# Kernel optimization log

Measured on AMD Instinct MI355X. Metric: run time of the kernel, lower is better.

The kernel has to match this reference:

```python
import jax, jax.numpy as jnp
import numpy as np

EPS = 1e-12


def _phi(e):
    # e: [C, L] -> pairwise euclidean distances [C, C], diagonal zeroed
    sq = jnp.sum(e * e, axis=1)                      # [C]
    prod = e @ e.T                                   # [C, C]
    d2 = sq[:, None] + sq[None, :] - 2.0 * prod
    d = jnp.sqrt(jnp.clip(d2, EPS, None))
    C = e.shape[0]
    return d * (1.0 - jnp.eye(C, dtype=e.dtype))


def setup_inputs() -> dict:
    key = jax.random.key(0)
    k1, k2, k3 = jax.random.split(key, 3)
    N, C, L = 64, 512, 256
    le_student = jax.random.normal(k1, (N, C, L), dtype=jnp.float32)
    le_teacher = jax.random.normal(k2, (N, C, L), dtype=jnp.float32)
    targets = jax.random.randint(k3, (N, C), 0, 2, dtype=jnp.int32)
    return {"le_student": le_student, "le_teacher": le_teacher, "targets": targets}


def reference(le_student, le_teacher, targets):
    N, C, L = le_student.shape
    m = targets.astype(le_student.dtype)             # [N, C] 0/1 mask
    es = le_student * m[:, :, None]                  # zero out negative rows
    et = le_teacher * m[:, :, None]

    Ds = jax.vmap(_phi)(es)                          # [N, C, C]
    Dt = jax.vmap(_phi)(et)                          # [N, C, C]

    eye = jnp.eye(C, dtype=m.dtype)
    pm = m[:, :, None] * m[:, None, :]               # pairs of positive rows
    offdiag = pm * (1.0 - eye)                       # off-diagonal positive pairs

    npos = jnp.sum(m, axis=1)                        # [N]
    cnt = npos * (npos - 1.0)                        # entries with d > 0 in submatrix
    valid = npos > 1.0
    safe_cnt = jnp.maximum(cnt, 1.0)

    mean_s = jnp.sum(Ds * offdiag, axis=(1, 2)) / safe_cnt
    mean_t = jax.lax.stop_gradient(jnp.sum(Dt * offdiag, axis=(1, 2)) / safe_cnt)
    mean_s = jnp.where(valid, mean_s, 1.0)
    mean_t = jnp.where(valid, mean_t, 1.0)

    d = Ds / mean_s[:, None, None]
    td = jax.lax.stop_gradient(Dt / mean_t[:, None, None])

    diff = d - td
    adiff = jnp.abs(diff)
    huber = jnp.where(adiff < 1.0, 0.5 * diff * diff, adiff - 0.5)

    per = jnp.sum(huber * pm, axis=(1, 2)) / jnp.maximum(npos, 1.0)
    return jnp.sum(jnp.where(valid, per, 0.0))
```

## Files before the change

kernel.cpp:

```cpp
#include <hip/hip_runtime.h>
#include <hip/hip_bf16.h>
#include <hip/hip_fp16.h>
#include <math.h>

#define NB 64
#define CC 512
#define LL 256

typedef __attribute__((ext_vector_type(4))) float floatx4;
typedef __attribute__((ext_vector_type(8))) short short8;

static __device__ __forceinline__ unsigned f2bf2(float x, float y) {
    __hip_bfloat162 h = __float22bfloat162_rn(make_float2(x, y));
    union { __hip_bfloat162 h; unsigned u; } c; c.h = h;
    return c.u;
}
static __device__ __forceinline__ unsigned f2h(float x) {
    __half h = __float2half_rn(x);
    union { __half h; unsigned short u; } c; c.h = h;
    return (unsigned)c.u;
}
static __device__ __forceinline__ float h2f(unsigned u) {
    union { unsigned short u; __half h; } c; c.u = (unsigned short)u;
    return __half2float(c.h);
}

__global__ __launch_bounds__(256) void dist_kernel(
    const float* __restrict__ S, const float* __restrict__ T,
    const int* __restrict__ targets,
    float* __restrict__ psumS, float* __restrict__ psumT,
    int* __restrict__ npos_ws, unsigned* __restrict__ D,
    float* __restrict__ out)
{
    const int bx = blockIdx.x;
    const int n = bx & (NB - 1), lin = bx >> 6;
    int tI = 0, rem = lin;
    while (rem >= 8 - tI) { rem -= 8 - tI; ++tI; }
    const int tJ = tI + rem;
    const bool diag = (tI == tJ);

    __shared__ int s_idx[CC];
    __shared__ int s_cnt[8], s_off[8];
    __shared__ int s_npS;
    __shared__ __align__(16) unsigned short lds[4][64][40];
    __shared__ float s_norm[4][64];
    __shared__ float redA[4], redB[4];

    const int tid = threadIdx.x;
    const int w = tid >> 6, lane = tid & 63;

    const int* tg = targets + n * CC;
    const bool p0 = tg[tid] != 0;
    const bool p1 = tg[tid + 256] != 0;
    const unsigned long long m0 = __ballot(p0);
    const unsigned long long m1 = __ballot(p1);
    if (lane == 0) { s_cnt[w] = __popcll(m0); s_cnt[4 + w] = __popcll(m1); }
    __syncthreads();
    if (tid == 0) {
        int a = 0;
        for (int i = 0; i < 8; ++i) { s_off[i] = a; a += s_cnt[i]; }
        s_npS = a;
    }
    __syncthreads();
    const unsigned long long below = (1ull << lane) - 1ull;
    if (p0) s_idx[s_off[w] + __popcll(m0 & below)] = tid;
    if (p1) s_idx[s_off[4 + w] + __popcll(m1 & below)] = tid + 256;
    __syncthreads();
    const int np = s_npS;

    if (tid == 0 && lin == 0) {
        npos_ws[n] = np;
        if (n == 0) out[0] = 0.0f;
    }

    const bool work = (np >= 2) && (tI * 64 < np) && (tJ * 64 < np);

    float t0 = 0.0f, t1 = 0.0f;
    if (work) {
        const bool stager = (!diag) || ((w & 1) == 0);
        const char* Pbase = (const char*)(((w >> 1) ? T : S) + (size_t)n * CC * LL);
        const int tileBase = ((w & 1) ? tJ : tI) * 64;
        const int r8 = lane >> 3, c8 = lane & 7;
        unsigned off_[8];
        #pragma unroll
        for (int i = 0; i < 8; ++i) {
            const int gk = tileBase + r8 + 8 * i;
            const int row = s_idx[(gk < np) ? gk : 0];
            off_[i] = (unsigned)(row * LL * 4 + c8 * 16);
        }

        float4 pre[8];
        float nprt[8];
        #pragma unroll
        for (int i = 0; i < 8; ++i) nprt[i] = 0.0f;
        if (stager) {
            #pragma unroll
            for (int i = 0; i < 8; ++i) pre[i] = *(const float4*)(Pbase + off_[i]);
        }

        const int m16 = lane & 15, quad = lane >> 4;
        const int bufB = diag ? 0 : 1;
        const int wrow = w * 16;

        floatx4 accS[4], accT[4];
        #pragma unroll
        for (int c = 0; c < 4; ++c) {
            accS[c][0] = 0; accS[c][1] = 0; accS[c][2] = 0; accS[c][3] = 0;
            accT[c][0] = 0; accT[c][1] = 0; accT[c][2] = 0; accT[c][3] = 0;
        }

        for (int kk = 0; kk < 8; ++kk) {
            __syncthreads();
            if (stager) {
                #pragma unroll
                for (int i = 0; i < 8; ++i) {
                    nprt[i] += pre[i].x * pre[i].x + pre[i].y * pre[i].y +
                               pre[i].z * pre[i].z + pre[i].w * pre[i].w;
                    *(uint2*)&lds[w][r8 + 8 * i][c8 * 4] =
                        make_uint2(f2bf2(pre[i].x, pre[i].y), f2bf2(pre[i].z, pre[i].w));
                }
            }
            __syncthreads();
            if (stager && kk < 7) {
                #pragma unroll
                for (int i = 0; i < 8; ++i)
                    pre[i] = *(const float4*)(Pbase + off_[i] + (kk + 1) * 128);
            }
            const int aoff = (wrow + m16) * 40 + quad * 8;
            const short8 a_s = *(const short8*)(&lds[0][0][0] + aoff);
            const short8 a_t = *(const short8*)(&lds[2][0][0] + aoff);
            #pragma unroll
            for (int c = 0; c < 4; ++c) {
                const int boff = (c * 16 + m16) * 40 + quad * 8;
                const short8 b_s = *(const short8*)(&lds[bufB][0][0] + boff);
                const short8 b_t = *(const short8*)(&lds[2 + bufB][0][0] + boff);
                accS[c] = __builtin_amdgcn_mfma_f32_16x16x32_bf16(a_s, b_s, accS[c], 0, 0, 0);
                accT[c] = __builtin_amdgcn_mfma_f32_16x16x32_bf16(a_t, b_t, accT[c], 0, 0, 0);
            }
        }

        if (stager) {
            #pragma unroll
            for (int i = 0; i < 8; ++i) {
                float v = nprt[i];
                v += __shfl_xor(v, 1); v += __shfl_xor(v, 2); v += __shfl_xor(v, 4);
                if (c8 == 0) s_norm[w][r8 + 8 * i] = v;
            }
        }
        __syncthreads();

        unsigned* Dn = D + ((size_t)bx << 12);
        float l0 = 0.0f, l1 = 0.0f;
        #pragma unroll
        for (int c = 0; c < 4; ++c) {
            const int colL = c * 16 + m16;
            const int gj = tJ * 64 + colL;
            const float nBs = s_norm[bufB][colL];
            const float nBt = s_norm[2 + bufB][colL];
            #pragma unroll
            for (int r = 0; r < 4; ++r) {
                const int rowL = wrow + quad * 4 + r;
                const int gi = tI * 64 + rowL;
                const float ds = sqrtf(fmaxf(s_norm[0][rowL] + nBs - 2.0f * accS[c][r], 1e-12f));
                const float dt = sqrtf(fmaxf(s_norm[2][rowL] + nBt - 2.0f * accT[c][r], 1e-12f));
                if (gi < np && gj < np && gi != gj) { l0 += ds; l1 += dt; }
                Dn[rowL * 64 + colL] = f2h(ds) | (f2h(dt) << 16);
            }
        }

        #pragma unroll
        for (int o = 32; o; o >>= 1) { l0 += __shfl_down(l0, o); l1 += __shfl_down(l1, o); }
        if (lane == 0) { redA[w] = l0; redB[w] = l1; }
        __syncthreads();
        if (tid == 0) {
            const float wgt = diag ? 1.0f : 2.0f;
            t0 = wgt * (redA[0] + redA[1] + redA[2] + redA[3]);
            t1 = wgt * (redB[0] + redB[1] + redB[2] + redB[3]);
        }
    }
    if (tid == 0) { psumS[bx] = t0; psumT[bx] = t1; }
}

__global__ __launch_bounds__(256) void huber_kernel(
    const unsigned* __restrict__ D, const int* __restrict__ npos,
    const float* __restrict__ psumS, const float* __restrict__ psumT,
    float* __restrict__ out)
{
    const int bx = blockIdx.x;
    const int n = bx & (NB - 1), lin = bx >> 6;
    int tI = 0, rem = lin;
    while (rem >= 8 - tI) { rem -= 8 - tI; ++tI; }
    const int tJ = tI + rem;

    const int np = npos[n];
    if (np < 2) return;
    if (tI * 64 >= np || tJ * 64 >= np) return;

    float ss = 0.0f, st = 0.0f;
    #pragma unroll
    for (int t = 0; t < 36; ++t) { ss += psumS[t * 64 + n]; st += psumT[t * 64 + n]; }
    const float cnt = (float)np * (float)(np - 1);
    const float inv_ms = cnt / ss;
    const float inv_mt = cnt / st;

    const uint4* Dn = (const uint4*)(D + ((size_t)bx << 12));
    const int tid = threadIdx.x;

    float h = 0.0f;
    #pragma unroll
    for (int it = 0; it < 4; ++it) {
        const int e4 = it * 256 + tid;
        const uint4 v = Dn[e4];
        const unsigned vv[4] = { v.x, v.y, v.z, v.w };
        const int e0 = e4 * 4;
        #pragma unroll
        for (int k = 0; k < 4; ++k) {
            const int e = e0 + k;
            const int gi = tI * 64 + (e >> 6);
            const int gj = tJ * 64 + (e & 63);
            if (gi < np && gj < np && gi != gj) {
                const float ds = h2f(vv[k] & 0xffffu);
                const float dt = h2f(vv[k] >> 16);
                const float diff = ds * inv_ms - dt * inv_mt;
                const float ad = fabsf(diff);
                h += (ad < 1.0f) ? 0.5f * diff * diff : ad - 0.5f;
            }
        }
    }

    #pragma unroll
    for (int o = 32; o; o >>= 1) h += __shfl_down(h, o);
    __shared__ float red[4];
    const int w = tid >> 6, lane = tid & 63;
    if (lane == 0) red[w] = h;
    __syncthreads();
    if (tid == 0) {
        const float wgt = (tI == tJ) ? 1.0f : 2.0f;
        atomicAdd(out, wgt * (red[0] + red[1] + red[2] + red[3]) / (float)np);
    }
}

extern "C" void kernel_launch(void* const* d_in, const int* in_sizes, int n_in,
                              void* d_out, int out_size, void* d_ws, size_t ws_size,
                              hipStream_t stream) {
    const float* S = (const float*)d_in[0];
    const float* T = (const float*)d_in[1];
    const int* targets = (const int*)d_in[2];
    float* out = (float*)d_out;

    float* psumS = (float*)d_ws;
    float* psumT = psumS + 2304;
    int* npos_ws = (int*)(psumT + 2304);
    size_t off = ((size_t)((char*)(npos_ws + 64) - (char*)d_ws) + 255) & ~(size_t)255;
    unsigned* D = (unsigned*)((char*)d_ws + off);

    dist_kernel<<<NB * 36, 256, 0, stream>>>(S, T, targets, psumS, psumT, npos_ws, D, out);
    huber_kernel<<<NB * 36, 256, 0, stream>>>(D, npos_ws, psumS, psumT, out);
}
```

Before: 133.3 us.

## Add prep pass compacting positive rows to bf16 and use smaller 32x32 tiles

A new prep kernel gathers the positive rows, converts them to a packed bf16 array, and precomputes row norms once per batch. The distance kernel then reads operands for 32x32 tiles straight from global memory with one wave per block, instead of restaging fp32 rows into LDS for every 64x64 tile. Per-batch mean sums now accumulate through atomics rather than a partial-sum array scan. The price is an extra launch, a round trip of the compacted bf16 copy through memory, and four times as many smaller blocks.

```diff
diff --git a/kernel.cpp b/kernel.cpp
--- a/kernel.cpp
+++ b/kernel.cpp
@@ -25,26 +25,18 @@
     return __half2float(c.h);
 }
 
-__global__ __launch_bounds__(256) void dist_kernel(
+__global__ __launch_bounds__(256) void prep_kernel(
     const float* __restrict__ S, const float* __restrict__ T,
     const int* __restrict__ targets,
-    float* __restrict__ psumS, float* __restrict__ psumT,
-    int* __restrict__ npos_ws, unsigned* __restrict__ D,
-    float* __restrict__ out)
+    int* __restrict__ idx, int* __restrict__ npos,
+    float* __restrict__ sumS, float* __restrict__ sumT, float* __restrict__ out,
+    unsigned short* __restrict__ Ps, unsigned short* __restrict__ Pt,
+    float* __restrict__ ns, float* __restrict__ nt)
 {
-    const int bx = blockIdx.x;
-    const int n = bx & (NB - 1), lin = bx >> 6;
-    int tI = 0, rem = lin;
-    while (rem >= 8 - tI) { rem -= 8 - tI; ++tI; }
-    const int tJ = tI + rem;
-    const bool diag = (tI == tJ);
-
+    const int g = blockIdx.x, n = blockIdx.y;
     __shared__ int s_idx[CC];
     __shared__ int s_cnt[8], s_off[8];
     __shared__ int s_npS;
-    __shared__ __align__(16) unsigned short lds[4][64][40];
-    __shared__ float s_norm[4][64];
-    __shared__ float redA[4], redB[4];
 
     const int tid = threadIdx.x;
     const int w = tid >> 6, lane = tid & 63;
@@ -68,156 +60,172 @@
     __syncthreads();
     const int np = s_npS;
 
-    if (tid == 0 && lin == 0) {
-        npos_ws[n] = np;
-        if (n == 0) out[0] = 0.0f;
-    }
-
-    const bool work = (np >= 2) && (tI * 64 < np) && (tJ * 64 < np);
-
-    float t0 = 0.0f, t1 = 0.0f;
-    if (work) {
-        const bool stager = (!diag) || ((w & 1) == 0);
-        const char* Pbase = (const char*)(((w >> 1) ? T : S) + (size_t)n * CC * LL);
-        const int tileBase = ((w & 1) ? tJ : tI) * 64;
-        const int r8 = lane >> 3, c8 = lane & 7;
-        unsigned off_[8];
-        #pragma unroll
-        for (int i = 0; i < 8; ++i) {
-            const int gk = tileBase + r8 + 8 * i;
-            const int row = s_idx[(gk < np) ? gk : 0];
-            off_[i] = (unsigned)(row * LL * 4 + c8 * 16);
-        }
-
-        float4 pre[8];
-        float nprt[8];
-        #pragma unroll
-        for (int i = 0; i < 8; ++i) nprt[i] = 0.0f;
-        if (stager) {
-            #pragma unroll
-            for (int i = 0; i < 8; ++i) pre[i] = *(const float4*)(Pbase + off_[i]);
-        }
-
-        const int m16 = lane & 15, quad = lane >> 4;
-        const int bufB = diag ? 0 : 1;
-        const int wrow = w * 16;
-
-        floatx4 accS[4], accT[4];
-        #pragma unroll
-        for (int c = 0; c < 4; ++c) {
-            accS[c][0] = 0; accS[c][1] = 0; accS[c][2] = 0; accS[c][3] = 0;
-            accT[c][0] = 0; accT[c][1] = 0; accT[c][2] = 0; accT[c][3] = 0;
-        }
-
-        for (int kk = 0; kk < 8; ++kk) {
-            __syncthreads();
-            if (stager) {
-                #pragma unroll
-                for (int i = 0; i < 8; ++i) {
-                    nprt[i] += pre[i].x * pre[i].x + pre[i].y * pre[i].y +
-                               pre[i].z * pre[i].z + pre[i].w * pre[i].w;
-                    *(uint2*)&lds[w][r8 + 8 * i][c8 * 4] =
-                        make_uint2(f2bf2(pre[i].x, pre[i].y), f2bf2(pre[i].z, pre[i].w));
-                }
-            }
-            __syncthreads();
-            if (stager && kk < 7) {
-                #pragma unroll
-                for (int i = 0; i < 8; ++i)
-                    pre[i] = *(const float4*)(Pbase + off_[i] + (kk + 1) * 128);
-            }
-            const int aoff = (wrow + m16) * 40 + quad * 8;
-            const short8 a_s = *(const short8*)(&lds[0][0][0] + aoff);
-            const short8 a_t = *(const short8*)(&lds[2][0][0] + aoff);
-            #pragma unroll
-            for (int c = 0; c < 4; ++c) {
-                const int boff = (c * 16 + m16) * 40 + quad * 8;
-                const short8 b_s = *(const short8*)(&lds[bufB][0][0] + boff);
-                const short8 b_t = *(const short8*)(&lds[2 + bufB][0][0] + boff);
-                accS[c] = __builtin_amdgcn_mfma_f32_16x16x32_bf16(a_s, b_s, accS[c], 0, 0, 0);
-                accT[c] = __builtin_amdgcn_mfma_f32_16x16x32_bf16(a_t, b_t, accT[c], 0, 0, 0);
-            }
-        }
-
-        if (stager) {
-            #pragma unroll
-            for (int i = 0; i < 8; ++i) {
-                float v = nprt[i];
-                v += __shfl_xor(v, 1); v += __shfl_xor(v, 2); v += __shfl_xor(v, 4);
-                if (c8 == 0) s_norm[w][r8 + 8 * i] = v;
-            }
-        }
-        __syncthreads();
-
-        unsigned* Dn = D + ((size_t)bx << 12);
-        float l0 = 0.0f, l1 = 0.0f;
-        #pragma unroll
-        for (int c = 0; c < 4; ++c) {
-            const int colL = c * 16 + m16;
-            const int gj = tJ * 64 + colL;
-            const float nBs = s_norm[bufB][colL];
-            const float nBt = s_norm[2 + bufB][colL];
+    if (g == 0) {
+        for (int k = tid; k < np; k += 256) idx[n * CC + k] = s_idx[k];
+        if (tid == 0) {
+            npos[n] = np;
+            sumS[n] = 0.0f; sumT[n] = 0.0f;
+            if (n == 0) out[0] = 0.0f;
+        }
+    }
+
+    const int kend = min(np, (g + 1) * 64);
+    for (int k = g * 64 + w; k < kend; k += 4) {
+        const int r = s_idx[k];
+        const float4 a = ((const float4*)(S + ((size_t)n * CC + r) * LL))[lane];
+        const float4 b = ((const float4*)(T + ((size_t)n * CC + r) * LL))[lane];
+        const size_t dst = ((size_t)n * CC + k) * LL + lane * 4;
+        *(uint2*)&Ps[dst] = make_uint2(f2bf2(a.x, a.y), f2bf2(a.z, a.w));
+        *(uint2*)&Pt[dst] = make_uint2(f2bf2(b.x, b.y), f2bf2(b.z, b.w));
+        float vs = a.x * a.x + a.y * a.y + a.z * a.z + a.w * a.w;
+        float vt = b.x * b.x + b.y * b.y + b.z * b.z + b.w * b.w;
+        #pragma unroll
+        for (int o = 32; o; o >>= 1) { vs += __shfl_down(vs, o); vt += __shfl_down(vt, o); }
+        if (lane == 0) { ns[n * CC + k] = vs; nt[n * CC + k] = vt; }
+    }
+}
+
+__global__ __launch_bounds__(64) void dist_kernel(
+    const unsigned short* __restrict__ Ps, const unsigned short* __restrict__ Pt,
+    const float* __restrict__ ns, const float* __restrict__ nt,
+    const int* __restrict__ npos,
+    float* __restrict__ sumS, float* __restrict__ sumT,
+    unsigned* __restrict__ D)
+{
+    const int bx = blockIdx.x;
+    const int n = bx & (NB - 1), lin = bx >> 6;
+    int tI = 0, rem = lin;
+    while (rem >= 16 - tI) { rem -= 16 - tI; ++tI; }
+    const int tJ = tI + rem;
+    const bool diag = (tI == tJ);
+
+    const int np = npos[n];
+    if (np < 2 || tI * 32 >= np || tJ * 32 >= np) return;
+
+    const int lane = threadIdx.x;
+    const int m16 = lane & 15, quad = lane >> 4;
+
+    const int rA0 = min(tI * 32 + m16, np - 1);
+    const int rA1 = min(tI * 32 + 16 + m16, np - 1);
+    const int rB0 = min(tJ * 32 + m16, np - 1);
+    const int rB1 = min(tJ * 32 + 16 + m16, np - 1);
+    const size_t base = (size_t)n * CC * LL + quad * 8;
+    const unsigned short* a0s = Ps + base + (size_t)rA0 * LL;
+    const unsigned short* a1s = Ps + base + (size_t)rA1 * LL;
+    const unsigned short* b0s = Ps + base + (size_t)rB0 * LL;
+    const unsigned short* b1s = Ps + base + (size_t)rB1 * LL;
+    const unsigned short* a0t = Pt + base + (size_t)rA0 * LL;
+    const unsigned short* a1t = Pt + base + (size_t)rA1 * LL;
+    const unsigned short* b0t = Pt + base + (size_t)rB0 * LL;
+    const unsigned short* b1t = Pt + base + (size_t)rB1 * LL;
+
+    floatx4 accS[4], accT[4];
+    #pragma unroll
+    for (int q = 0; q < 4; ++q) {
+        accS[q][0] = 0; accS[q][1] = 0; accS[q][2] = 0; accS[q][3] = 0;
+        accT[q][0] = 0; accT[q][1] = 0; accT[q][2] = 0; accT[q][3] = 0;
+    }
+
+    #pragma unroll 2
+    for (int kk = 0; kk < 8; ++kk) {
+        const int o = kk * 32;
+        const short8 fa0s = *(const short8*)(a0s + o);
+        const short8 fa1s = *(const short8*)(a1s + o);
+        const short8 fb0s = *(const short8*)(b0s + o);
+        const short8 fb1s = *(const short8*)(b1s + o);
+        const short8 fa0t = *(const short8*)(a0t + o);
+        const short8 fa1t = *(const short8*)(a1t + o);
+        const short8 fb0t = *(const short8*)(b0t + o);
+        const short8 fb1t = *(const short8*)(b1t + o);
+        accS[0] = __builtin_amdgcn_mfma_f32_16x16x32_bf16(fa0s, fb0s, accS[0], 0, 0, 0);
+        accS[1] = __builtin_amdgcn_mfma_f32_16x16x32_bf16(fa0s, fb1s, accS[1], 0, 0, 0);
+        accS[2] = __builtin_amdgcn_mfma_f32_16x16x32_bf16(fa1s, fb0s, accS[2], 0, 0, 0);
+        accS[3] = __builtin_amdgcn_mfma_f32_16x16x32_bf16(fa1s, fb1s, accS[3], 0, 0, 0);
+        accT[0] = __builtin_amdgcn_mfma_f32_16x16x32_bf16(fa0t, fb0t, accT[0], 0, 0, 0);
+        accT[1] = __builtin_amdgcn_mfma_f32_16x16x32_bf16(fa0t, fb1t, accT[1], 0, 0, 0);
+        accT[2] = __builtin_amdgcn_mfma_f32_16x16x32_bf16(fa1t, fb0t, accT[2], 0, 0, 0);
+        accT[3] = __builtin_amdgcn_mfma_f32_16x16x32_bf16(fa1t, fb1t, accT[3], 0, 0, 0);
+    }
+
+    float nsR[8], ntR[8];
+    #pragma unroll
+    for (int qi = 0; qi < 2; ++qi)
+        #pragma unroll
+        for (int r = 0; r < 4; ++r) {
+            const int gi = min(tI * 32 + qi * 16 + quad * 4 + r, np - 1);
+            nsR[qi * 4 + r] = ns[n * CC + gi];
+            ntR[qi * 4 + r] = nt[n * CC + gi];
+        }
+    float nsC[2], ntC[2];
+    #pragma unroll
+    for (int qj = 0; qj < 2; ++qj) {
+        const int gj = min(tJ * 32 + qj * 16 + m16, np - 1);
+        nsC[qj] = ns[n * CC + gj];
+        ntC[qj] = nt[n * CC + gj];
+    }
+
+    unsigned* Dn = D + ((size_t)bx << 10);
+    float l0 = 0.0f, l1 = 0.0f;
+    #pragma unroll
+    for (int qi = 0; qi < 2; ++qi)
+        #pragma unroll
+        for (int qj = 0; qj < 2; ++qj) {
+            const int q = qi * 2 + qj;
+            const int colL = qj * 16 + m16;
+            const int gj = tJ * 32 + colL;
             #pragma unroll
             for (int r = 0; r < 4; ++r) {
-                const int rowL = wrow + quad * 4 + r;
-                const int gi = tI * 64 + rowL;
-                const float ds = sqrtf(fmaxf(s_norm[0][rowL] + nBs - 2.0f * accS[c][r], 1e-12f));
-                const float dt = sqrtf(fmaxf(s_norm[2][rowL] + nBt - 2.0f * accT[c][r], 1e-12f));
+                const int rowL = qi * 16 + quad * 4 + r;
+                const int gi = tI * 32 + rowL;
+                const float ds = sqrtf(fmaxf(nsR[qi * 4 + r] + nsC[qj] - 2.0f * accS[q][r], 1e-12f));
+                const float dt = sqrtf(fmaxf(ntR[qi * 4 + r] + ntC[qj] - 2.0f * accT[q][r], 1e-12f));
                 if (gi < np && gj < np && gi != gj) { l0 += ds; l1 += dt; }
-                Dn[rowL * 64 + colL] = f2h(ds) | (f2h(dt) << 16);
+                Dn[rowL * 32 + colL] = f2h(ds) | (f2h(dt) << 16);
             }
         }
 
-        #pragma unroll
-        for (int o = 32; o; o >>= 1) { l0 += __shfl_down(l0, o); l1 += __shfl_down(l1, o); }
-        if (lane == 0) { redA[w] = l0; redB[w] = l1; }
-        __syncthreads();
-        if (tid == 0) {
-            const float wgt = diag ? 1.0f : 2.0f;
-            t0 = wgt * (redA[0] + redA[1] + redA[2] + redA[3]);
-            t1 = wgt * (redB[0] + redB[1] + redB[2] + redB[3]);
-        }
-    }
-    if (tid == 0) { psumS[bx] = t0; psumT[bx] = t1; }
-}
-
-__global__ __launch_bounds__(256) void huber_kernel(
+    #pragma unroll
+    for (int o = 32; o; o >>= 1) { l0 += __shfl_down(l0, o); l1 += __shfl_down(l1, o); }
+    if (lane == 0) {
+        const float wgt = diag ? 1.0f : 2.0f;
+        atomicAdd(&sumS[n], wgt * l0);
+        atomicAdd(&sumT[n], wgt * l1);
+    }
+}
+
+__global__ __launch_bounds__(64) void huber_kernel(
     const unsigned* __restrict__ D, const int* __restrict__ npos,
-    const float* __restrict__ psumS, const float* __restrict__ psumT,
+    const float* __restrict__ sumS, const float* __restrict__ sumT,
     float* __restrict__ out)
 {
     const int bx = blockIdx.x;
     const int n = bx & (NB - 1), lin = bx >> 6;
     int tI = 0, rem = lin;
-    while (rem >= 8 - tI) { rem -= 8 - tI; ++tI; }
+    while (rem >= 16 - tI) { rem -= 16 - tI; ++tI; }
     const int tJ = tI + rem;
 
     const int np = npos[n];
-    if (np < 2) return;
-    if (tI * 64 >= np || tJ * 64 >= np) return;
-
-    float ss = 0.0f, st = 0.0f;
-    #pragma unroll
-    for (int t = 0; t < 36; ++t) { ss += psumS[t * 64 + n]; st += psumT[t * 64 + n]; }
+    if (np < 2 || tI * 32 >= np || tJ * 32 >= np) return;
+
     const float cnt = (float)np * (float)(np - 1);
-    const float inv_ms = cnt / ss;
-    const float inv_mt = cnt / st;
-
-    const uint4* Dn = (const uint4*)(D + ((size_t)bx << 12));
-    const int tid = threadIdx.x;
+    const float inv_ms = cnt / sumS[n];
+    const float inv_mt = cnt / sumT[n];
+
+    const uint4* Dn = (const uint4*)(D + ((size_t)bx << 10));
+    const int lane = threadIdx.x;
 
     float h = 0.0f;
     #pragma unroll
     for (int it = 0; it < 4; ++it) {
-        const int e4 = it * 256 + tid;
+        const int e4 = it * 64 + lane;
         const uint4 v = Dn[e4];
         const unsigned vv[4] = { v.x, v.y, v.z, v.w };
         const int e0 = e4 * 4;
         #pragma unroll
         for (int k = 0; k < 4; ++k) {
             const int e = e0 + k;
-            const int gi = tI * 64 + (e >> 6);
-            const int gj = tJ * 64 + (e & 63);
+            const int gi = tI * 32 + (e >> 5);
+            const int gj = tJ * 32 + (e & 31);
             if (gi < np && gj < np && gi != gj) {
                 const float ds = h2f(vv[k] & 0xffffu);
                 const float dt = h2f(vv[k] >> 16);
@@ -230,13 +238,9 @@
 
     #pragma unroll
     for (int o = 32; o; o >>= 1) h += __shfl_down(h, o);
-    __shared__ float red[4];
-    const int w = tid >> 6, lane = tid & 63;
-    if (lane == 0) red[w] = h;
-    __syncthreads();
-    if (tid == 0) {
+    if (lane == 0) {
         const float wgt = (tI == tJ) ? 1.0f : 2.0f;
-        atomicAdd(out, wgt * (red[0] + red[1] + red[2] + red[3]) / (float)np);
+        atomicAdd(out, wgt * h / (float)np);
     }
 }
 
@@ -248,12 +252,21 @@
     const int* targets = (const int*)d_in[2];
     float* out = (float*)d_out;
 
-    float* psumS = (float*)d_ws;
-    float* psumT = psumS + 2304;
-    int* npos_ws = (int*)(psumT + 2304);
-    size_t off = ((size_t)((char*)(npos_ws + 64) - (char*)d_ws) + 255) & ~(size_t)255;
-    unsigned* D = (unsigned*)((char*)d_ws + off);
-
-    dist_kernel<<<NB * 36, 256, 0, stream>>>(S, T, targets, psumS, psumT, npos_ws, D, out);
-    huber_kernel<<<NB * 36, 256, 0, stream>>>(D, npos_ws, psumS, psumT, out);
-}
+    char* p = (char*)d_ws;
+    int* idx = (int*)p;                  p += (size_t)NB * CC * 4;
+    int* npos = (int*)p;                 p += NB * 4;
+    float* sumS = (float*)p;             p += NB * 4;
+    float* sumT = (float*)p;             p += NB * 4;
+    float* ns = (float*)p;               p += (size_t)NB * CC * 4;
+    float* nt = (float*)p;               p += (size_t)NB * CC * 4;
+    p = (char*)(((size_t)p + 255) & ~(size_t)255);
+    unsigned short* Ps = (unsigned short*)p;  p += (size_t)NB * CC * LL * 2;
+    unsigned short* Pt = (unsigned short*)p;  p += (size_t)NB * CC * LL * 2;
+    unsigned* D = (unsigned*)p;
+
+    prep_kernel<<<dim3(8, NB), 256, 0, stream>>>(S, T, targets, idx, npos,
+                                                 sumS, sumT, out, Ps, Pt, ns, nt);
+    const int nblk = 136 * NB;
+    dist_kernel<<<nblk, 64, 0, stream>>>(Ps, Pt, ns, nt, npos, sumS, sumT, D);
+    huber_kernel<<<nblk, 64, 0, stream>>>(D, npos, sumS, sumT, out);
+}
```

Result: slower. 177.4 us (+33.1%).

## Split index compaction into prep kernel, double-buffer LDS, use atomic per-sample sums

Applied to the files above, without the earlier changes.

Moves the per-sample positive-row compaction out of every dist block into a small prep kernel that writes indices to global memory. Dist blocks are now grouped per sample and tiles beyond the positive count exit early through a tile decode on the actual tile count. The LDS staging becomes double-buffered, which drops one barrier per k-step. Per-sample distance sums are accumulated with atomics instead of partial arrays summed in the huber kernel. The cost is an extra kernel launch, more LDS per block, and nondeterministic float atomic ordering.

```diff
diff --git a/kernel.cpp b/kernel.cpp
--- a/kernel.cpp
+++ b/kernel.cpp
@@ -25,30 +25,14 @@
     return __half2float(c.h);
 }
 
-__global__ __launch_bounds__(256) void dist_kernel(
-    const float* __restrict__ S, const float* __restrict__ T,
+__global__ __launch_bounds__(256) void prep_kernel(
     const int* __restrict__ targets,
-    float* __restrict__ psumS, float* __restrict__ psumT,
-    int* __restrict__ npos_ws, unsigned* __restrict__ D,
-    float* __restrict__ out)
+    int* __restrict__ idx, int* __restrict__ npos,
+    float* __restrict__ sumS, float* __restrict__ sumT, float* __restrict__ out)
 {
-    const int bx = blockIdx.x;
-    const int n = bx & (NB - 1), lin = bx >> 6;
-    int tI = 0, rem = lin;
-    while (rem >= 8 - tI) { rem -= 8 - tI; ++tI; }
-    const int tJ = tI + rem;
-    const bool diag = (tI == tJ);
-
-    __shared__ int s_idx[CC];
+    const int n = blockIdx.x, tid = threadIdx.x;
     __shared__ int s_cnt[8], s_off[8];
-    __shared__ int s_npS;
-    __shared__ __align__(16) unsigned short lds[4][64][40];
-    __shared__ float s_norm[4][64];
-    __shared__ float redA[4], redB[4];
-
-    const int tid = threadIdx.x;
     const int w = tid >> 6, lane = tid & 63;
-
     const int* tg = targets + n * CC;
     const bool p0 = tg[tid] != 0;
     const bool p1 = tg[tid + 256] != 0;
@@ -59,149 +43,162 @@
     if (tid == 0) {
         int a = 0;
         for (int i = 0; i < 8; ++i) { s_off[i] = a; a += s_cnt[i]; }
-        s_npS = a;
+        npos[n] = a;
+        sumS[n] = 0.0f; sumT[n] = 0.0f;
+        if (n == 0) out[0] = 0.0f;
     }
     __syncthreads();
     const unsigned long long below = (1ull << lane) - 1ull;
-    if (p0) s_idx[s_off[w] + __popcll(m0 & below)] = tid;
-    if (p1) s_idx[s_off[4 + w] + __popcll(m1 & below)] = tid + 256;
-    __syncthreads();
-    const int np = s_npS;
-
-    if (tid == 0 && lin == 0) {
-        npos_ws[n] = np;
-        if (n == 0) out[0] = 0.0f;
-    }
-
-    const bool work = (np >= 2) && (tI * 64 < np) && (tJ * 64 < np);
-
-    float t0 = 0.0f, t1 = 0.0f;
-    if (work) {
-        const bool stager = (!diag) || ((w & 1) == 0);
-        const char* Pbase = (const char*)(((w >> 1) ? T : S) + (size_t)n * CC * LL);
-        const int tileBase = ((w & 1) ? tJ : tI) * 64;
-        const int r8 = lane >> 3, c8 = lane & 7;
-        unsigned off_[8];
-        #pragma unroll
-        for (int i = 0; i < 8; ++i) {
-            const int gk = tileBase + r8 + 8 * i;
-            const int row = s_idx[(gk < np) ? gk : 0];
-            off_[i] = (unsigned)(row * LL * 4 + c8 * 16);
-        }
-
-        float4 pre[8];
-        float nprt[8];
-        #pragma unroll
-        for (int i = 0; i < 8; ++i) nprt[i] = 0.0f;
-        if (stager) {
-            #pragma unroll
-            for (int i = 0; i < 8; ++i) pre[i] = *(const float4*)(Pbase + off_[i]);
-        }
-
-        const int m16 = lane & 15, quad = lane >> 4;
-        const int bufB = diag ? 0 : 1;
-        const int wrow = w * 16;
-
-        floatx4 accS[4], accT[4];
-        #pragma unroll
-        for (int c = 0; c < 4; ++c) {
-            accS[c][0] = 0; accS[c][1] = 0; accS[c][2] = 0; accS[c][3] = 0;
-            accT[c][0] = 0; accT[c][1] = 0; accT[c][2] = 0; accT[c][3] = 0;
-        }
-
-        for (int kk = 0; kk < 8; ++kk) {
-            __syncthreads();
-            if (stager) {
-                #pragma unroll
-                for (int i = 0; i < 8; ++i) {
-                    nprt[i] += pre[i].x * pre[i].x + pre[i].y * pre[i].y +
-                               pre[i].z * pre[i].z + pre[i].w * pre[i].w;
-                    *(uint2*)&lds[w][r8 + 8 * i][c8 * 4] =
-                        make_uint2(f2bf2(pre[i].x, pre[i].y), f2bf2(pre[i].z, pre[i].w));
-                }
-            }
-            __syncthreads();
-            if (stager && kk < 7) {
-                #pragma unroll
-                for (int i = 0; i < 8; ++i)
-                    pre[i] = *(const float4*)(Pbase + off_[i] + (kk + 1) * 128);
-            }
-            const int aoff = (wrow + m16) * 40 + quad * 8;
-            const short8 a_s = *(const short8*)(&lds[0][0][0] + aoff);
-            const short8 a_t = *(const short8*)(&lds[2][0][0] + aoff);
-            #pragma unroll
-            for (int c = 0; c < 4; ++c) {
-                const int boff = (c * 16 + m16) * 40 + quad * 8;
-                const short8 b_s = *(const short8*)(&lds[bufB][0][0] + boff);
-                const short8 b_t = *(const short8*)(&lds[2 + bufB][0][0] + boff);
-                accS[c] = __builtin_amdgcn_mfma_f32_16x16x32_bf16(a_s, b_s, accS[c], 0, 0, 0);
-                accT[c] = __builtin_amdgcn_mfma_f32_16x16x32_bf16(a_t, b_t, accT[c], 0, 0, 0);
-            }
-        }
-
+    if (p0) idx[n * CC + s_off[w] + __popcll(m0 & below)] = tid;
+    if (p1) idx[n * CC + s_off[4 + w] + __popcll(m1 & below)] = tid + 256;
+}
+
+static __device__ __forceinline__ bool decode_tile(int t, int u, int& tI, int& tJ) {
+    if (t >= (u * (u + 1)) >> 1) return false;
+    tI = 0;
+    while (t >= u - tI) { t -= u - tI; ++tI; }
+    tJ = tI + t;
+    return true;
+}
+
+__global__ __launch_bounds__(256) void dist_kernel(
+    const float* __restrict__ S, const float* __restrict__ T,
+    const int* __restrict__ idx, const int* __restrict__ npos,
+    float* __restrict__ sumS, float* __restrict__ sumT,
+    unsigned* __restrict__ D)
+{
+    const int bx = blockIdx.x;
+    const int n = bx / 36;
+    const int np = npos[n];
+    if (np < 2) return;
+    int tI, tJ;
+    if (!decode_tile(bx - n * 36, (np + 63) >> 6, tI, tJ)) return;
+    const bool diag = (tI == tJ);
+
+    __shared__ __align__(16) unsigned short lds[4][2][64][40];
+    __shared__ float s_norm[4][64];
+    __shared__ float redA[4], redB[4];
+
+    const int tid = threadIdx.x;
+    const int w = tid >> 6, lane = tid & 63;
+
+    const bool stager = (!diag) || ((w & 1) == 0);
+    const char* Pbase = (const char*)(((w >> 1) ? T : S) + (size_t)n * CC * LL);
+    const int tileBase = ((w & 1) ? tJ : tI) * 64;
+    const int r8 = lane >> 3, c8 = lane & 7;
+    unsigned off_[8];
+    #pragma unroll
+    for (int i = 0; i < 8; ++i) {
+        const int gk = tileBase + r8 + 8 * i;
+        const int row = idx[n * CC + ((gk < np) ? gk : 0)];
+        off_[i] = (unsigned)(row * LL * 4 + c8 * 16);
+    }
+
+    float4 pre[8];
+    float nprt[8];
+    #pragma unroll
+    for (int i = 0; i < 8; ++i) nprt[i] = 0.0f;
+    if (stager) {
+        #pragma unroll
+        for (int i = 0; i < 8; ++i) pre[i] = *(const float4*)(Pbase + off_[i]);
+    }
+
+    const int m16 = lane & 15, quad = lane >> 4;
+    const int bufB = diag ? 0 : 1;
+    const int wrow = w * 16;
+
+    floatx4 accS[4], accT[4];
+    #pragma unroll
+    for (int c = 0; c < 4; ++c) {
+        accS[c][0] = 0; accS[c][1] = 0; accS[c][2] = 0; accS[c][3] = 0;
+        accT[c][0] = 0; accT[c][1] = 0; accT[c][2] = 0; accT[c][3] = 0;
+    }
+
+    for (int kk = 0; kk < 8; ++kk) {
+        const int pb = kk & 1;
         if (stager) {
             #pragma unroll
             for (int i = 0; i < 8; ++i) {
-                float v = nprt[i];
-                v += __shfl_xor(v, 1); v += __shfl_xor(v, 2); v += __shfl_xor(v, 4);
-                if (c8 == 0) s_norm[w][r8 + 8 * i] = v;
+                nprt[i] += pre[i].x * pre[i].x + pre[i].y * pre[i].y +
+                           pre[i].z * pre[i].z + pre[i].w * pre[i].w;
+                *(uint2*)&lds[w][pb][r8 + 8 * i][c8 * 4] =
+                    make_uint2(f2bf2(pre[i].x, pre[i].y), f2bf2(pre[i].z, pre[i].w));
             }
         }
         __syncthreads();
-
-        unsigned* Dn = D + ((size_t)bx << 12);
-        float l0 = 0.0f, l1 = 0.0f;
+        if (stager && kk < 7) {
+            #pragma unroll
+            for (int i = 0; i < 8; ++i)
+                pre[i] = *(const float4*)(Pbase + off_[i] + (kk + 1) * 128);
+        }
+        const int aoff = (wrow + m16) * 40 + quad * 8;
+        const short8 a_s = *(const short8*)(&lds[0][pb][0][0] + aoff);
+        const short8 a_t = *(const short8*)(&lds[2][pb][0][0] + aoff);
         #pragma unroll
         for (int c = 0; c < 4; ++c) {
-            const int colL = c * 16 + m16;
-            const int gj = tJ * 64 + colL;
-            const float nBs = s_norm[bufB][colL];
-            const float nBt = s_norm[2 + bufB][colL];
-            #pragma unroll
-            for (int r = 0; r < 4; ++r) {
-                const int rowL = wrow + quad * 4 + r;
-                const int gi = tI * 64 + rowL;
-                const float ds = sqrtf(fmaxf(s_norm[0][rowL] + nBs - 2.0f * accS[c][r], 1e-12f));
-                const float dt = sqrtf(fmaxf(s_norm[2][rowL] + nBt - 2.0f * accT[c][r], 1e-12f));
-                if (gi < np && gj < np && gi != gj) { l0 += ds; l1 += dt; }
-                Dn[rowL * 64 + colL] = f2h(ds) | (f2h(dt) << 16);
-            }
-        }
-
-        #pragma unroll
-        for (int o = 32; o; o >>= 1) { l0 += __shfl_down(l0, o); l1 += __shfl_down(l1, o); }
-        if (lane == 0) { redA[w] = l0; redB[w] = l1; }
-        __syncthreads();
-        if (tid == 0) {
-            const float wgt = diag ? 1.0f : 2.0f;
-            t0 = wgt * (redA[0] + redA[1] + redA[2] + redA[3]);
-            t1 = wgt * (redB[0] + redB[1] + redB[2] + redB[3]);
-        }
-    }
-    if (tid == 0) { psumS[bx] = t0; psumT[bx] = t1; }
+            const int boff = (c * 16 + m16) * 40 + quad * 8;
+            const short8 b_s = *(const short8*)(&lds[bufB][pb][0][0] + boff);
+            const short8 b_t = *(const short8*)(&lds[2 + bufB][pb][0][0] + boff);
+            accS[c] = __builtin_amdgcn_mfma_f32_16x16x32_bf16(a_s, b_s, accS[c], 0, 0, 0);
+            accT[c] = __builtin_amdgcn_mfma_f32_16x16x32_bf16(a_t, b_t, accT[c], 0, 0, 0);
+        }
+    }
+
+    if (stager) {
+        #pragma unroll
+        for (int i = 0; i < 8; ++i) {
+            float v = nprt[i];
+            v += __shfl_xor(v, 1); v += __shfl_xor(v, 2); v += __shfl_xor(v, 4);
+            if (c8 == 0) s_norm[w][r8 + 8 * i] = v;
+        }
+    }
+    __syncthreads();
+
+    unsigned* Dn = D + ((size_t)bx << 12);
+    float l0 = 0.0f, l1 = 0.0f;
+    #pragma unroll
+    for (int c = 0; c < 4; ++c) {
+        const int colL = c * 16 + m16;
+        const int gj = tJ * 64 + colL;
+        const float nBs = s_norm[bufB][colL];
+        const float nBt = s_norm[2 + bufB][colL];
+        #pragma unroll
+        for (int r = 0; r < 4; ++r) {
+            const int rowL = wrow + quad * 4 + r;
+            const int gi = tI * 64 + rowL;
+            const float ds = sqrtf(fmaxf(s_norm[0][rowL] + nBs - 2.0f * accS[c][r], 1e-12f));
+            const float dt = sqrtf(fmaxf(s_norm[2][rowL] + nBt - 2.0f * accT[c][r], 1e-12f));
+            if (gi < np && gj < np && gi != gj) { l0 += ds; l1 += dt; }
+            Dn[rowL * 64 + colL] = f2h(ds) | (f2h(dt) << 16);
+        }
+    }
+
+    #pragma unroll
+    for (int o = 32; o; o >>= 1) { l0 += __shfl_down(l0, o); l1 += __shfl_down(l1, o); }
+    if (lane == 0) { redA[w] = l0; redB[w] = l1; }
+    __syncthreads();
+    if (tid == 0) {
+        const float wgt = diag ? 1.0f : 2.0f;
+        atomicAdd(&sumS[n], wgt * (redA[0] + redA[1] + redA[2] + redA[3]));
+        atomicAdd(&sumT[n], wgt * (redB[0] + redB[1] + redB[2] + redB[3]));
+    }
 }
 
 __global__ __launch_bounds__(256) void huber_kernel(
     const unsigned* __restrict__ D, const int* __restrict__ npos,
-    const float* __restrict__ psumS, const float* __restrict__ psumT,
+    const float* __restrict__ sumS, const float* __restrict__ sumT,
     float* __restrict__ out)
 {
     const int bx = blockIdx.x;
-    const int n = bx & (NB - 1), lin = bx >> 6;
-    int tI = 0, rem = lin;
-    while (rem >= 8 - tI) { rem -= 8 - tI; ++tI; }
-    const int tJ = tI + rem;
-
+    const int n = bx / 36;
     const int np = npos[n];
     if (np < 2) return;
-    if (tI * 64 >= np || tJ * 64 >= np) return;
-
-    float ss = 0.0f, st = 0.0f;
-    #pragma unroll
-    for (int t = 0; t < 36; ++t) { ss += psumS[t * 64 + n]; st += psumT[t * 64 + n]; }
+    int tI, tJ;
+    if (!decode_tile(bx - n * 36, (np + 63) >> 6, tI, tJ)) return;
+
     const float cnt = (float)np * (float)(np - 1);
-    const float inv_ms = cnt / ss;
-    const float inv_mt = cnt / st;
+    const float inv_ms = cnt / sumS[n];
+    const float inv_mt = cnt / sumT[n];
 
     const uint4* Dn = (const uint4*)(D + ((size_t)bx << 12));
     const int tid = threadIdx.x;
@@ -248,12 +245,15 @@
     const int* targets = (const int*)d_in[2];
     float* out = (float*)d_out;
 
-    float* psumS = (float*)d_ws;
-    float* psumT = psumS + 2304;
-    int* npos_ws = (int*)(psumT + 2304);
-    size_t off = ((size_t)((char*)(npos_ws + 64) - (char*)d_ws) + 255) & ~(size_t)255;
-    unsigned* D = (unsigned*)((char*)d_ws + off);
-
-    dist_kernel<<<NB * 36, 256, 0, stream>>>(S, T, targets, psumS, psumT, npos_ws, D, out);
-    huber_kernel<<<NB * 36, 256, 0, stream>>>(D, npos_ws, psumS, psumT, out);
-}
+    char* p = (char*)d_ws;
+    int* idx = (int*)p;        p += (size_t)NB * CC * 4;
+    int* npos = (int*)p;       p += NB * 4;
+    float* sumS = (float*)p;   p += NB * 4;
+    float* sumT = (float*)p;   p += NB * 4;
+    p = (char*)(((size_t)p + 255) & ~(size_t)255);
+    unsigned* D = (unsigned*)p;
+
+    prep_kernel<<<NB, 256, 0, stream>>>(targets, idx, npos, sumS, sumT, out);
+    dist_kernel<<<NB * 36, 256, 0, stream>>>(S, T, idx, npos, sumS, sumT, D);
+    huber_kernel<<<NB * 36, 256, 0, stream>>>(D, npos, sumS, sumT, out);
+}
```

Measured after the change: 137.4 us. +3.1%, slower.
